# Optimization experiments

Hardware: AMD Instinct MI355X
Metric: run time of the kernel (lower is better)

The kernel has to match this reference:

```python
import jax, jax.numpy as jnp
import numpy as np

S_IN = 14; KERNEL = 3; STRIDE = 1; C_IN = 32; C_OUT = 32; BATCH = 4; ROUTINGS = 3
EPS = 1e-7

def _child_parent_map(size_in, kernel, stride):
    # Same construction as BaseCaps._generate_voting_map: for each output position,
    # the flattened indices of its kernel window in the size_in x size_in grid.
    rows = []
    for row in range(0, size_in - kernel + 1, stride):
        for col in range(0, size_in - kernel + 1, stride):
            w = []
            for kr in range(kernel):
                start = (row + kr) * size_in + col
                w.extend(range(start, start + kernel))
            rows.append(w)
    return np.array(rows, dtype=np.int32)  # [size_out^2, kernel^2]

def setup_inputs() -> dict:
    key = jax.random.key(0)
    ks = jax.random.split(key, 5)
    in_act = jax.random.uniform(ks[0], (BATCH, S_IN, S_IN, C_IN, 1), jnp.float32)
    in_pose = jax.random.normal(ks[1], (BATCH, S_IN, S_IN, C_IN, 4, 4), jnp.float32)
    W = jax.random.normal(ks[2], (KERNEL * KERNEL * C_IN, C_OUT, 4, 4), jnp.float32) * 0.1
    beta_v = jax.random.normal(ks[3], (C_OUT,), jnp.float32)
    beta_a = jax.random.normal(ks[4], (C_OUT,), jnp.float32)
    cpm = jnp.asarray(_child_parent_map(S_IN, KERNEL, STRIDE))
    return {"in_act": in_act, "in_pose": in_pose, "transformation_weights": W,
            "beta_a": beta_a, "beta_v": beta_v, "child_parent_map": cpm}

def em_routing(act, votes, beta_a, beta_v, routings):
    # act: [B,P,K,1,1]  votes: [B,P,K,C,16]
    B, P, K, C, D = votes.shape
    rr = jnp.full((B, P, K, C, 1), 1.0 / C, votes.dtype)
    it_min, it_max = 1.0, max(1.0, min(float(routings), 3.0))
    out_a = out_mu = None
    for i in range(routings):
        inv_temp = it_min + (it_max - it_min) * (i / max(1.0, routings - 1.0))
        # --- M-step ---
        rp = rr * act                                        # [B,P,K,C,1]
        rs = rp.sum(axis=2, keepdims=True) + EPS             # [B,P,1,C,1]
        mu = (rp * votes).sum(axis=2, keepdims=True) / rs    # [B,P,1,C,D]
        var = (rp * (votes - mu) ** 2).sum(axis=2, keepdims=True) / rs + EPS
        cost = (beta_v[:, None] + 0.5 * jnp.log(var)) * rs   # [B,P,1,C,D]
        out_a = jax.nn.sigmoid(inv_temp * (beta_a[:, None] - cost.sum(-1, keepdims=True)))
        # --- E-step ---
        if i < routings - 1:
            log_p = -0.5 * jnp.sum(jnp.log(2.0 * jnp.pi * var) + (votes - mu) ** 2 / var,
                                   axis=-1, keepdims=True)   # [B,P,K,C,1]
            rr = jax.nn.softmax(jnp.log(out_a + EPS) + log_p, axis=3)
        out_mu = mu
    return out_a[:, :, 0, :, 0], out_mu[:, :, 0]  # [B,P,C], [B,P,C,D]

def reference(in_act, in_pose, transformation_weights, beta_a, beta_v, child_parent_map):
    B, S, _, Cin, _ = in_act.shape
    P, Kw = child_parent_map.shape           # [out_spatial^2, kernel^2]
    Sout = int(round(P ** 0.5))
    C = transformation_weights.shape[1]
    act = in_act.reshape(B, S * S, Cin)
    pose = in_pose.reshape(B, S * S, Cin, 4, 4)
    # gather kernel windows of child capsules per output position
    act_g = act[:, child_parent_map].reshape(B, P, Kw * Cin)             # [B,P,K]
    pose_g = pose[:, child_parent_map].reshape(B, P, Kw * Cin, 4, 4)     # [B,P,K,4,4]
    # votes = child_pose @ W, per (child k, parent capsule c)
    votes = jnp.einsum('bpkij,kcjl->bpkcil', pose_g, transformation_weights)
    votes = votes.reshape(B, P, Kw * Cin, C, 16)
    out_a, out_mu = em_routing(act_g[..., None, None], votes, beta_a, beta_v, ROUTINGS)
    out_act = out_a.reshape(B, Sout, Sout, C, 1)
    out_pose = out_mu.reshape(B, Sout, Sout, C, 4, 4)
    return out_act, out_pose
```

## Files before the change

kernel.cpp:

```cpp
#include <hip/hip_runtime.h>
#include <math.h>

#define NB 4
#define NP 144
#define KW 9
#define CIN 32
#define NC 32
#define NK 288
#define ND 16
#define NDH 8
#define EPSI 1e-7f
#define NT 512
#define KPT 18
#define NRED 4


typedef float v2f __attribute__((ext_vector_type(2)));

__device__ __forceinline__ v2f mkv2(float a, float b) { v2f r; r[0] = a; r[1] = b; return r; }

template<int CTRL>
__device__ __forceinline__ float dppf(float x) {
    return __int_as_float(__builtin_amdgcn_update_dpp(
        0, __float_as_int(x), CTRL, 0xF, 0xF, true));
}
__device__ __forceinline__ float swz16(float x) {
    return __int_as_float(__builtin_amdgcn_ds_swizzle(__float_as_int(x), 0x401F));
}
__device__ __forceinline__ float red32_max(float x) {
    x = fmaxf(x, dppf<0xB1>(x));
    x = fmaxf(x, dppf<0x4E>(x));
    x = fmaxf(x, dppf<0x141>(x));
    x = fmaxf(x, dppf<0x140>(x));
    x = fmaxf(x, swz16(x));
    return x;
}
__device__ __forceinline__ float red32_sum(float x) {
    x += dppf<0xB1>(x);
    x += dppf<0x4E>(x);
    x += dppf<0x141>(x);
    x += dppf<0x140>(x);
    x += swz16(x);
    return x;
}
__device__ __forceinline__ float red16_sum(float x) {
    x += dppf<0xB1>(x);
    x += dppf<0x4E>(x);
    x += dppf<0x141>(x);
    x += dppf<0x140>(x);
    return x;
}

__device__ __forceinline__ int sw4(int c, int j) { return j ^ ((c >> 1) & 3); }

__device__ __forceinline__ void load16(const float* src, float* dst) {
    const float4* s4 = (const float4*)src;
    *(float4*)&dst[0]  = s4[0];
    *(float4*)&dst[4]  = s4[1];
    *(float4*)&dst[8]  = s4[2];
    *(float4*)&dst[12] = s4[3];
}
__device__ __forceinline__ void load16v(const float* src, v2f* dst) {
    const float4* s4 = (const float4*)src;
    #pragma unroll
    for (int q = 0; q < 4; ++q) {
        const float4 tq = s4[q];
        dst[q*2+0] = mkv2(tq.x, tq.y);
        dst[q*2+1] = mkv2(tq.z, tq.w);
    }
}

__device__ __forceinline__ void vote44v(const float* pr, const v2f* wr2, v2f* v2) {
    #pragma unroll
    for (int i = 0; i < 4; ++i) {
        const v2f p0 = mkv2(pr[i*4+0], pr[i*4+0]);
        const v2f p1 = mkv2(pr[i*4+1], pr[i*4+1]);
        const v2f p2 = mkv2(pr[i*4+2], pr[i*4+2]);
        const v2f p3 = mkv2(pr[i*4+3], pr[i*4+3]);
        #pragma unroll
        for (int p = 0; p < 2; ++p) {
            v2f acc = p0 * wr2[0*2+p];
            acc += p1 * wr2[1*2+p];
            acc += p2 * wr2[2*2+p];
            acc += p3 * wr2[3*2+p];
            v2[i*2+p] = acc;
        }
    }
}

__device__ __forceinline__ void estep_body(
    const v2f v2[NDH], float actk,
    const v2f iv2v[NDH], const v2f h2n2v[NDH], float A2,
    float& r0, v2f m1v[NDH], v2f m2v[NDH])
{
    v2f q2v = mkv2(0.0f, 0.0f);
    #pragma unroll
    for (int e = 0; e < NDH; ++e)
        q2v += (iv2v[e] * v2[e] + h2n2v[e]) * v2[e];
    const float logit2 = A2 - (q2v[0] + q2v[1]);

    const float mx = red32_max(logit2);
    const float e  = __builtin_amdgcn_exp2f(logit2 - mx);
    const float se = red32_sum(e);
    const float rp = e * __builtin_amdgcn_rcpf(se) * actk;
    r0 += rp;
    const v2f rpv = mkv2(rp, rp);
    #pragma unroll
    for (int d = 0; d < NDH; ++d) {
        const v2f rv = rpv * v2[d];
        m1v[d] += rv;
        m2v[d] += rv * v2[d];
    }
}

__device__ __forceinline__ void pass0_body(
    const v2f v2[NDH], float actk,
    float& r0, v2f m1v[NDH], v2f m2v[NDH])
{
    const float rp = actk * (1.0f / 32.0f);
    r0 += rp;
    const v2f rpv = mkv2(rp, rp);
    #pragma unroll
    for (int d = 0; d < NDH; ++d) {
        const v2f rv = rpv * v2[d];
        m1v[d] += rv;
        m2v[d] += rv * v2[d];
    }
}

__device__ __forceinline__ void reduce_finalize(
    float r0, float m1[ND], float m2[ND],
    int t, int c, int wave, int lane, float inv_temp, bool last,
    float rbeta_a, float rbeta_v,
    float (&s_m1)[NRED][NC][ND], float (&s_m2)[NRED][NC][ND], float (&s_r0)[NRED][NC],
    float (&s_mu)[NC][17], float (&s_ivar)[NC][17], float (&s_A)[NC])
{
    r0 += __shfl_xor(r0, 32);
    #pragma unroll
    for (int d = 0; d < ND; ++d) {
        m1[d] += __shfl_xor(m1[d], 32);
        m2[d] += __shfl_xor(m2[d], 32);
    }
    if (lane < 32 && wave >= NRED) {
        float4* d1 = (float4*)&s_m1[wave - NRED][c][0];
        float4* d2 = (float4*)&s_m2[wave - NRED][c][0];
        #pragma unroll
        for (int j = 0; j < 4; ++j) {
            d1[sw4(c, j)] = *(const float4*)&m1[4*j];
            d2[sw4(c, j)] = *(const float4*)&m2[4*j];
        }
        s_r0[wave - NRED][c] = r0;
    }
    __syncthreads();
    if (lane < 32 && wave < NRED) {
        float4* d1 = (float4*)&s_m1[wave][c][0];
        float4* d2 = (float4*)&s_m2[wave][c][0];
        #pragma unroll
        for (int j = 0; j < 4; ++j) {
            float4 v1 = d1[sw4(c, j)];
            v1.x += m1[4*j]; v1.y += m1[4*j+1]; v1.z += m1[4*j+2]; v1.w += m1[4*j+3];
            d1[sw4(c, j)] = v1;
            float4 v2 = d2[sw4(c, j)];
            v2.x += m2[4*j]; v2.y += m2[4*j+1]; v2.z += m2[4*j+2]; v2.w += m2[4*j+3];
            d2[sw4(c, j)] = v2;
        }
        s_r0[wave][c] += r0;
    }
    __syncthreads();

    {
        const int cc = t >> 4;
        const int d  = t & 15;
        const int fi = cc * ND + sw4(cc, d >> 2) * 4 + (d & 3);
        float am1 = 0.0f, am2 = 0.0f, ar0 = 0.0f;
        #pragma unroll
        for (int g = 0; g < NRED; ++g) {
            am1 += (&s_m1[g][0][0])[fi];
            am2 += (&s_m2[g][0][0])[fi];
            ar0 += s_r0[g][cc];
        }
        const float rs  = ar0 + EPSI;
        const float irs = __builtin_amdgcn_rcpf(rs);
        const float mu  = am1 * irs;
        const float var = (am2 - mu * (2.0f * am1 - mu * ar0)) * irs + EPSI;
        const float lv  = __logf(var);
        s_mu[cc][d]   = mu;
        s_ivar[cc][d] = __builtin_amdgcn_rcpf(var);
        const float Ls = red16_sum(lv);
        if (d == 0) s_A[cc] = Ls;
    }
    __syncthreads();

    if (t < NC) {
        const float log2pi16 = 16.0f * 1.8378770664093453f;
        float ar0 = s_r0[0][t] + s_r0[1][t] + s_r0[2][t] + s_r0[3][t];
        const float rs = ar0 + EPSI;
        const float L  = s_A[t];
        const float costsum = rs * (16.0f * rbeta_v + 0.5f * L);
        const float x  = inv_temp * (rbeta_a - costsum);
        const float oa = 1.0f / (1.0f + __expf(-x));
        s_A[t] = last ? oa : (__logf(oa + EPSI) - 0.5f * (log2pi16 + L));
    }
    __syncthreads();
}

__global__ __launch_bounds__(NT) void convcaps_em_kernel(
    const float* __restrict__ g_act,
    const float* __restrict__ g_pose,
    const float* __restrict__ g_W,
    const float* __restrict__ g_beta_a,
    const float* __restrict__ g_beta_v,
    const int*   __restrict__ g_cpm,
    float* __restrict__ g_out)
{
    __shared__ float s_pose[NK][ND];
    __shared__ float s_act[NK];
    __shared__ float s_m1[NRED][NC][ND];
    __shared__ float s_m2[NRED][NC][ND];
    __shared__ float s_r0[NRED][NC];
    __shared__ float s_mu[NC][17];
    __shared__ float s_ivar[NC][17];
    __shared__ float s_A[NC];

    const int bp   = blockIdx.x;
    const int b    = bp / NP;
    const int p    = bp - b * NP;
    const int t    = threadIdx.x;
    const int c    = t & 31;
    const int s    = t >> 5;
    const int wave = t >> 6;
    const int lane = t & 63;

    float rbeta_a = 0.0f, rbeta_v = 0.0f;
    if (t < NC) { rbeta_a = g_beta_a[t]; rbeta_v = g_beta_v[t]; }

    {
        const int* cpm = g_cpm + p * KW;
        const float4* pb4 = (const float4*)(g_pose + (size_t)b * (196 * CIN * ND));
        float4* sp4 = (float4*)&s_pose[0][0];
        #pragma unroll 1
        for (int i4 = t; i4 < NK * ND / 4; i4 += NT) {
            const int w   = i4 >> 7;
            const int rem = i4 & 127;
            sp4[i4] = pb4[(size_t)cpm[w] * 128 + rem];
        }
        const float* ab = g_act + (size_t)b * (196 * CIN);
        if (t < NK) s_act[t] = ab[cpm[t >> 5] * CIN + (t & 31)];
    }
    __syncthreads();

    const int    k0  = s * KPT;
    const float* wp0 = g_W + (size_t)(k0 * NC + c) * ND;

    {
        float r0 = 0.0f;
        v2f m1v[NDH], m2v[NDH];
        #pragma unroll
        for (int d = 0; d < NDH; ++d) { m1v[d] = mkv2(0,0); m2v[d] = mkv2(0,0); }

        v2f wrA[NDH], wrB[NDH];
        load16v(wp0, wrA);
        #pragma unroll 1
        for (int jj = 0; jj < KPT; jj += 2) {
            load16v(wp0 + (size_t)(jj + 1) * (NC * ND), wrB);
            {
                const float actk = s_act[k0 + jj];
                float pr[ND]; v2f v2[NDH];
                load16(&s_pose[k0 + jj][0], pr);
                vote44v(pr, wrA, v2);
                pass0_body(v2, actk, r0, m1v, m2v);
            }
            const int jn = (jj + 2 < KPT) ? (jj + 2) : (KPT - 1);
            load16v(wp0 + (size_t)jn * (NC * ND), wrA);
            {
                const float actk = s_act[k0 + jj + 1];
                float pr[ND]; v2f v2[NDH];
                load16(&s_pose[k0 + jj + 1][0], pr);
                vote44v(pr, wrB, v2);
                pass0_body(v2, actk, r0, m1v, m2v);
            }
        }
        float m1[ND], m2[ND];
        #pragma unroll
        for (int e = 0; e < NDH; ++e) {
            m1[2*e] = m1v[e][0]; m1[2*e+1] = m1v[e][1];
            m2[2*e] = m2v[e][0]; m2[2*e+1] = m2v[e][1];
        }
        reduce_finalize(r0, m1, m2, t, c, wave, lane, 1.0f, false, rbeta_a, rbeta_v,
                        s_m1, s_m2, s_r0, s_mu, s_ivar, s_A);
    }

    #pragma unroll 1
    for (int it = 1; it < 3; ++it) {
        const float L2E = 1.4426950408889634f;
        v2f iv2v[NDH], h2n2v[NDH];
        float gq2 = 0.0f;
        #pragma unroll
        for (int e = 0; e < NDH; ++e) {
            float ivs[2], hns[2];
            #pragma unroll
            for (int u = 0; u < 2; ++u) {
                const float mu  = s_mu[c][2*e+u];
                const float iv2 = s_ivar[c][2*e+u] * (0.5f * L2E);
                ivs[u] = iv2;
                const float h = iv2 * mu;
                hns[u] = -(h + h);
                gq2 = fmaf(h, mu, gq2);
            }
            iv2v[e]  = mkv2(ivs[0], ivs[1]);
            h2n2v[e] = mkv2(hns[0], hns[1]);
        }
        const float A2 = fmaf(L2E, s_A[c], -gq2);

        float r0 = 0.0f;
        v2f m1v[NDH], m2v[NDH];
        #pragma unroll
        for (int d = 0; d < NDH; ++d) { m1v[d] = mkv2(0,0); m2v[d] = mkv2(0,0); }

        v2f wrA[NDH], wrB[NDH];
        load16v(wp0, wrA);
        #pragma unroll 1
        for (int jj = 0; jj < KPT; jj += 2) {
            load16v(wp0 + (size_t)(jj + 1) * (NC * ND), wrB);
            {
                const float actk = s_act[k0 + jj];
                float pr[ND]; v2f v2[NDH];
                load16(&s_pose[k0 + jj][0], pr);
                vote44v(pr, wrA, v2);
                estep_body(v2, actk, iv2v, h2n2v, A2, r0, m1v, m2v);
            }
            const int jn = (jj + 2 < KPT) ? (jj + 2) : (KPT - 1);
            load16v(wp0 + (size_t)jn * (NC * ND), wrA);
            {
                const float actk = s_act[k0 + jj + 1];
                float pr[ND]; v2f v2[NDH];
                load16(&s_pose[k0 + jj + 1][0], pr);
                vote44v(pr, wrB, v2);
                estep_body(v2, actk, iv2v, h2n2v, A2, r0, m1v, m2v);
            }
        }
        float m1[ND], m2[ND];
        #pragma unroll
        for (int e = 0; e < NDH; ++e) {
            m1[2*e] = m1v[e][0]; m1[2*e+1] = m1v[e][1];
            m2[2*e] = m2v[e][0]; m2[2*e+1] = m2v[e][1];
        }
        reduce_finalize(r0, m1, m2, t, c, wave, lane, 1.0f + (float)it, it == 2,
                        rbeta_a, rbeta_v,
                        s_m1, s_m2, s_r0, s_mu, s_ivar, s_A);
    }

    const int base = (b * NP + p) * NC;
    if (t < NC) g_out[base + t] = s_A[t];
    float* outpose = g_out + NB * NP * NC;
    {
        const int cc = t >> 4;
        const int d  = t & 15;
        outpose[(size_t)(base + cc) * ND + d] = s_mu[cc][d];
    }
}

extern "C" void kernel_launch(void* const* d_in, const int* in_sizes, int n_in,
                              void* d_out, int out_size, void* d_ws, size_t ws_size,
                              hipStream_t stream) {
    const float* in_act  = (const float*)d_in[0];
    const float* in_pose = (const float*)d_in[1];
    const float* W       = (const float*)d_in[2];
    const float* beta_a  = (const float*)d_in[3];
    const float* beta_v  = (const float*)d_in[4];
    const int*   cpm     = (const int*)d_in[5];
    float* out = (float*)d_out;

    convcaps_em_kernel<<<dim3(NB * NP), dim3(NT), 0, stream>>>(
        in_act, in_pose, W, beta_a, beta_v, cpm, out);
}
```

Baseline: 101.2 us.

## Halve block size, process two children per step, merge softmax partials via online-max

The block shrinks from 512 to 256 threads, so each 32-lane group handles 36 children instead of 18 and the cross-wave reduction has two slots instead of four. The inner loop now computes votes for two children per iteration and interleaves their independent softmax reductions. Each 32-wide softmax is split into 16-lane DPP reductions followed by an online-max merge of the two halves through one swizzle, which aims to shorten the dependency chain. The weight-register double buffering is dropped, which lowers register pressure but exposes load latency and leaves half as many threads per block.

```diff
diff --git a/kernel.cpp b/kernel.cpp
--- a/kernel.cpp
+++ b/kernel.cpp
@@ -10,9 +10,9 @@
 #define ND 16
 #define NDH 8
 #define EPSI 1e-7f
-#define NT 512
-#define KPT 18
-#define NRED 4
+#define NT 256
+#define KPT 36
+#define NRED 2
 
 
 typedef float v2f __attribute__((ext_vector_type(2)));
@@ -27,20 +27,11 @@
 __device__ __forceinline__ float swz16(float x) {
     return __int_as_float(__builtin_amdgcn_ds_swizzle(__float_as_int(x), 0x401F));
 }
-__device__ __forceinline__ float red32_max(float x) {
+__device__ __forceinline__ float red16_max(float x) {
     x = fmaxf(x, dppf<0xB1>(x));
     x = fmaxf(x, dppf<0x4E>(x));
     x = fmaxf(x, dppf<0x141>(x));
     x = fmaxf(x, dppf<0x140>(x));
-    x = fmaxf(x, swz16(x));
-    return x;
-}
-__device__ __forceinline__ float red32_sum(float x) {
-    x += dppf<0xB1>(x);
-    x += dppf<0x4E>(x);
-    x += dppf<0x141>(x);
-    x += dppf<0x140>(x);
-    x += swz16(x);
     return x;
 }
 __device__ __forceinline__ float red16_sum(float x) {
@@ -88,53 +79,19 @@
     }
 }
 
-__device__ __forceinline__ void estep_body(
-    const v2f v2[NDH], float actk,
-    const v2f iv2v[NDH], const v2f h2n2v[NDH], float A2,
-    float& r0, v2f m1v[NDH], v2f m2v[NDH])
-{
-    v2f q2v = mkv2(0.0f, 0.0f);
-    #pragma unroll
-    for (int e = 0; e < NDH; ++e)
-        q2v += (iv2v[e] * v2[e] + h2n2v[e]) * v2[e];
-    const float logit2 = A2 - (q2v[0] + q2v[1]);
-
-    const float mx = red32_max(logit2);
-    const float e  = __builtin_amdgcn_exp2f(logit2 - mx);
-    const float se = red32_sum(e);
-    const float rp = e * __builtin_amdgcn_rcpf(se) * actk;
-    r0 += rp;
-    const v2f rpv = mkv2(rp, rp);
-    #pragma unroll
-    for (int d = 0; d < NDH; ++d) {
-        const v2f rv = rpv * v2[d];
-        m1v[d] += rv;
-        m2v[d] += rv * v2[d];
-    }
-}
-
-__device__ __forceinline__ void pass0_body(
-    const v2f v2[NDH], float actk,
-    float& r0, v2f m1v[NDH], v2f m2v[NDH])
-{
-    const float rp = actk * (1.0f / 32.0f);
-    r0 += rp;
-    const v2f rpv = mkv2(rp, rp);
-    #pragma unroll
-    for (int d = 0; d < NDH; ++d) {
-        const v2f rv = rpv * v2[d];
-        m1v[d] += rv;
-        m2v[d] += rv * v2[d];
-    }
-}
-
 __device__ __forceinline__ void reduce_finalize(
-    float r0, float m1[ND], float m2[ND],
+    float r0, v2f m1v[NDH], v2f m2v[NDH],
     int t, int c, int wave, int lane, float inv_temp, bool last,
     float rbeta_a, float rbeta_v,
     float (&s_m1)[NRED][NC][ND], float (&s_m2)[NRED][NC][ND], float (&s_r0)[NRED][NC],
     float (&s_mu)[NC][17], float (&s_ivar)[NC][17], float (&s_A)[NC])
 {
+    float m1[ND], m2[ND];
+    #pragma unroll
+    for (int e = 0; e < NDH; ++e) {
+        m1[2*e] = m1v[e][0]; m1[2*e+1] = m1v[e][1];
+        m2[2*e] = m2v[e][0]; m2[2*e+1] = m2v[e][1];
+    }
     r0 += __shfl_xor(r0, 32);
     #pragma unroll
     for (int d = 0; d < ND; ++d) {
@@ -168,17 +125,15 @@
     }
     __syncthreads();
 
-    {
-        const int cc = t >> 4;
-        const int d  = t & 15;
+    #pragma unroll
+    for (int m = 0; m < 2; ++m) {
+        const int item = t + m * NT;
+        const int cc = item >> 4;
+        const int d  = item & 15;
         const int fi = cc * ND + sw4(cc, d >> 2) * 4 + (d & 3);
-        float am1 = 0.0f, am2 = 0.0f, ar0 = 0.0f;
-        #pragma unroll
-        for (int g = 0; g < NRED; ++g) {
-            am1 += (&s_m1[g][0][0])[fi];
-            am2 += (&s_m2[g][0][0])[fi];
-            ar0 += s_r0[g][cc];
-        }
+        const float am1 = (&s_m1[0][0][0])[fi] + (&s_m1[1][0][0])[fi];
+        const float am2 = (&s_m2[0][0][0])[fi] + (&s_m2[1][0][0])[fi];
+        const float ar0 = s_r0[0][cc] + s_r0[1][cc];
         const float rs  = ar0 + EPSI;
         const float irs = __builtin_amdgcn_rcpf(rs);
         const float mu  = am1 * irs;
@@ -193,7 +148,7 @@
 
     if (t < NC) {
         const float log2pi16 = 16.0f * 1.8378770664093453f;
-        float ar0 = s_r0[0][t] + s_r0[1][t] + s_r0[2][t] + s_r0[3][t];
+        const float ar0 = s_r0[0][t] + s_r0[1][t];
         const float rs = ar0 + EPSI;
         const float L  = s_A[t];
         const float costsum = rs * (16.0f * rbeta_v + 0.5f * L);
@@ -244,8 +199,9 @@
             const int rem = i4 & 127;
             sp4[i4] = pb4[(size_t)cpm[w] * 128 + rem];
         }
-        const float* ab = g_act + (size_t)b * (196 * CIN);
-        if (t < NK) s_act[t] = ab[cpm[t >> 5] * CIN + (t & 31)];
+        #pragma unroll 1
+        for (int e = t; e < NK; e += NT)
+            s_act[e] = g_act[(size_t)b * (196 * CIN) + cpm[e >> 5] * CIN + (e & 31)];
     }
     __syncthreads();
 
@@ -258,35 +214,32 @@
         #pragma unroll
         for (int d = 0; d < NDH; ++d) { m1v[d] = mkv2(0,0); m2v[d] = mkv2(0,0); }
 
-        v2f wrA[NDH], wrB[NDH];
-        load16v(wp0, wrA);
+        const float* wp = wp0;
         #pragma unroll 1
-        for (int jj = 0; jj < KPT; jj += 2) {
-            load16v(wp0 + (size_t)(jj + 1) * (NC * ND), wrB);
-            {
-                const float actk = s_act[k0 + jj];
-                float pr[ND]; v2f v2[NDH];
-                load16(&s_pose[k0 + jj][0], pr);
-                vote44v(pr, wrA, v2);
-                pass0_body(v2, actk, r0, m1v, m2v);
+        for (int jj = 0; jj < KPT; jj += 2, wp += 2 * NC * ND) {
+            float pr[ND]; v2f wr[NDH];
+            v2f va[NDH], vb[NDH];
+            load16(&s_pose[k0 + jj][0], pr);
+            load16v(wp, wr);
+            vote44v(pr, wr, va);
+            load16(&s_pose[k0 + jj + 1][0], pr);
+            load16v(wp + NC * ND, wr);
+            vote44v(pr, wr, vb);
+
+            const float2 a2 = *(const float2*)&s_act[k0 + jj];
+            const float rpa = a2.x * (1.0f / 32.0f);
+            const float rpb = a2.y * (1.0f / 32.0f);
+            r0 += rpa + rpb;
+            const v2f rpav = mkv2(rpa, rpa), rpbv = mkv2(rpb, rpb);
+            #pragma unroll
+            for (int d = 0; d < NDH; ++d) {
+                const v2f rva = rpav * va[d];
+                const v2f rvb = rpbv * vb[d];
+                m1v[d] += rva + rvb;
+                m2v[d] += rva * va[d] + rvb * vb[d];
             }
-            const int jn = (jj + 2 < KPT) ? (jj + 2) : (KPT - 1);
-            load16v(wp0 + (size_t)jn * (NC * ND), wrA);
-            {
-                const float actk = s_act[k0 + jj + 1];
-                float pr[ND]; v2f v2[NDH];
-                load16(&s_pose[k0 + jj + 1][0], pr);
-                vote44v(pr, wrB, v2);
-                pass0_body(v2, actk, r0, m1v, m2v);
-            }
-        }
-        float m1[ND], m2[ND];
-        #pragma unroll
-        for (int e = 0; e < NDH; ++e) {
-            m1[2*e] = m1v[e][0]; m1[2*e+1] = m1v[e][1];
-            m2[2*e] = m2v[e][0]; m2[2*e+1] = m2v[e][1];
-        }
-        reduce_finalize(r0, m1, m2, t, c, wave, lane, 1.0f, false, rbeta_a, rbeta_v,
+        }
+        reduce_finalize(r0, m1v, m2v, t, c, wave, lane, 1.0f, false, rbeta_a, rbeta_v,
                         s_m1, s_m2, s_r0, s_mu, s_ivar, s_A);
     }
 
@@ -317,35 +270,58 @@
         #pragma unroll
         for (int d = 0; d < NDH; ++d) { m1v[d] = mkv2(0,0); m2v[d] = mkv2(0,0); }
 
-        v2f wrA[NDH], wrB[NDH];
-        load16v(wp0, wrA);
+        const float* wp = wp0;
         #pragma unroll 1
-        for (int jj = 0; jj < KPT; jj += 2) {
-            load16v(wp0 + (size_t)(jj + 1) * (NC * ND), wrB);
-            {
-                const float actk = s_act[k0 + jj];
-                float pr[ND]; v2f v2[NDH];
-                load16(&s_pose[k0 + jj][0], pr);
-                vote44v(pr, wrA, v2);
-                estep_body(v2, actk, iv2v, h2n2v, A2, r0, m1v, m2v);
+        for (int jj = 0; jj < KPT; jj += 2, wp += 2 * NC * ND) {
+            float pr[ND]; v2f wr[NDH];
+            v2f va[NDH], vb[NDH];
+            load16(&s_pose[k0 + jj][0], pr);
+            load16v(wp, wr);
+            vote44v(pr, wr, va);
+            load16(&s_pose[k0 + jj + 1][0], pr);
+            load16v(wp + NC * ND, wr);
+            vote44v(pr, wr, vb);
+
+            v2f qa2 = mkv2(0,0), qb2 = mkv2(0,0);
+            #pragma unroll
+            for (int e = 0; e < NDH; ++e) {
+                qa2 += (iv2v[e] * va[e] + h2n2v[e]) * va[e];
+                qb2 += (iv2v[e] * vb[e] + h2n2v[e]) * vb[e];
             }
-            const int jn = (jj + 2 < KPT) ? (jj + 2) : (KPT - 1);
-            load16v(wp0 + (size_t)jn * (NC * ND), wrA);
-            {
-                const float actk = s_act[k0 + jj + 1];
-                float pr[ND]; v2f v2[NDH];
-                load16(&s_pose[k0 + jj + 1][0], pr);
-                vote44v(pr, wrB, v2);
-                estep_body(v2, actk, iv2v, h2n2v, A2, r0, m1v, m2v);
+            const float la = A2 - (qa2[0] + qa2[1]);
+            const float lb = A2 - (qb2[0] + qb2[1]);
+
+            const float ma = red16_max(la);
+            const float mb = red16_max(lb);
+            const float ea = __builtin_amdgcn_exp2f(la - ma);
+            const float eb = __builtin_amdgcn_exp2f(lb - mb);
+            const float sa = red16_sum(ea);
+            const float sb = red16_sum(eb);
+            const float mao = swz16(ma);
+            const float sao = swz16(sa);
+            const float mbo = swz16(mb);
+            const float sbo = swz16(sb);
+            const float Ma = fmaxf(ma, mao);
+            const float Mb = fmaxf(mb, mbo);
+            const float wa = __builtin_amdgcn_exp2f(ma - Ma);
+            const float wb = __builtin_amdgcn_exp2f(mb - Mb);
+            const float Sa = fmaf(sao, __builtin_amdgcn_exp2f(mao - Ma), sa * wa);
+            const float Sb = fmaf(sbo, __builtin_amdgcn_exp2f(mbo - Mb), sb * wb);
+
+            const float2 a2 = *(const float2*)&s_act[k0 + jj];
+            const float rpa = ea * wa * __builtin_amdgcn_rcpf(Sa) * a2.x;
+            const float rpb = eb * wb * __builtin_amdgcn_rcpf(Sb) * a2.y;
+            r0 += rpa + rpb;
+            const v2f rpav = mkv2(rpa, rpa), rpbv = mkv2(rpb, rpb);
+            #pragma unroll
+            for (int d = 0; d < NDH; ++d) {
+                const v2f rva = rpav * va[d];
+                const v2f rvb = rpbv * vb[d];
+                m1v[d] += rva + rvb;
+                m2v[d] += rva * va[d] + rvb * vb[d];
             }
         }
-        float m1[ND], m2[ND];
-        #pragma unroll
-        for (int e = 0; e < NDH; ++e) {
-            m1[2*e] = m1v[e][0]; m1[2*e+1] = m1v[e][1];
-            m2[2*e] = m2v[e][0]; m2[2*e+1] = m2v[e][1];
-        }
-        reduce_finalize(r0, m1, m2, t, c, wave, lane, 1.0f + (float)it, it == 2,
+        reduce_finalize(r0, m1v, m2v, t, c, wave, lane, 1.0f + (float)it, it == 2,
                         rbeta_a, rbeta_v,
                         s_m1, s_m2, s_r0, s_mu, s_ivar, s_A);
     }
@@ -353,9 +329,11 @@
     const int base = (b * NP + p) * NC;
     if (t < NC) g_out[base + t] = s_A[t];
     float* outpose = g_out + NB * NP * NC;
-    {
-        const int cc = t >> 4;
-        const int d  = t & 15;
+    #pragma unroll
+    for (int m = 0; m < 2; ++m) {
+        const int item = t + m * NT;
+        const int cc = item >> 4;
+        const int d  = item & 15;
         outpose[(size_t)(base + cc) * ND + d] = s_mu[cc][d];
     }
 }
```

New measurement: 97.73 us. 3.4% less time.
